# Performance work log

Hardware: AMD Instinct MI355X
Metric: run time of the kernel (lower is better)

## Reference

```python
import jax, jax.numpy as jnp
import numpy as np

B, L, T, IN, H, OUT = 1024, 64, 128, 13, 64, 13
NEG = -1e30


def gru_step(x, h, Wih, Whh, bih, bhh):
    # PyTorch GRU cell: gates ordered (r, z, n)
    gi = x @ Wih.T + bih          # [B, 3H]
    gh = h @ Whh.T + bhh          # [B, 3H]
    ir, iz, inn = jnp.split(gi, 3, axis=-1)
    hr, hz, hn = jnp.split(gh, 3, axis=-1)
    r = jax.nn.sigmoid(ir + hr)
    z = jax.nn.sigmoid(iz + hz)
    n = jnp.tanh(inn + r * hn)
    return (1.0 - z) * n + z * h


def setup_inputs() -> dict:
    key = jax.random.key(0)
    ks = jax.random.split(key, 10)
    s = float(1.0 / np.sqrt(H))
    x = jax.random.normal(ks[0], (B, L, IN), jnp.float32)
    lengths = jax.random.randint(ks[1], (B,), 1, L + 1).at[0].set(L)
    Wih = jax.random.uniform(ks[2], (3 * H, IN), jnp.float32, -s, s)
    Whh = jax.random.uniform(ks[3], (3 * H, H), jnp.float32, -s, s)
    bih = jax.random.uniform(ks[4], (3 * H,), jnp.float32, -s, s)
    bhh = jax.random.uniform(ks[5], (3 * H,), jnp.float32, -s, s)
    Wf = jax.random.uniform(ks[6], (OUT, H), jnp.float32, -s, s)
    bf = jax.random.uniform(ks[7], (OUT,), jnp.float32, -s, s)
    Wa = jax.random.uniform(ks[8], (H, H), jnp.float32, -s, s)
    ba = jax.random.uniform(ks[9], (H,), jnp.float32, -s, s)
    return dict(x=x, lengths=lengths, output_length=T, Wih=Wih, Whh=Whh,
                bih=bih, bhh=bhh, Wf=Wf, bf=bf, Wa=Wa, ba=ba)


def reference(x, lengths, output_length, Wih, Whh, bih, bhh, Wf, bf, Wa, ba):
    b, l = x.shape[0], x.shape[1]
    xT = jnp.swapaxes(x, 0, 1)                        # [L, B, IN]
    h0 = jnp.zeros((b, H), x.dtype)

    # Encoder: masked GRU emulating pack_padded/pad_packed semantics:
    # hidden frozen past each sequence's length; outputs zero past length.
    def enc(h, inp):
        t, xt = inp
        hn = gru_step(xt, h, Wih, Whh, bih, bhh)
        valid = (t < lengths)[:, None]
        h = jnp.where(valid, hn, h)
        return h, jnp.where(valid, hn, 0.0)

    h, outs = jax.lax.scan(enc, h0, (jnp.arange(l), xT))
    # output[:, -1, :] of the padded output (zeros for seqs shorter than max)
    nin = outs[-1] @ Wf.T + bf                        # [B, OUT]

    Tn = output_length
    buf0 = jnp.zeros((Tn, b, H), x.dtype)             # growing past-prediction buffer

    def dec(carry, t):
        h, buf, nin = carry
        hn = gru_step(nin, h, Wih, Whh, bih, bhh)     # output_lstm == hidden (1 layer, 1 step)
        # attention recomputed over all past predictions (softmax over time axis)
        logits = jnp.einsum('tbh,gh->tbg', buf, Wa) + ba      # [T, B, H]
        logits = jnp.where((jnp.arange(Tn) < t)[:, None, None], logits, NEG)
        w = jax.nn.softmax(logits, axis=0)
        o = hn + jnp.sum(w * buf, axis=0)             # at t=0 buffer is all zeros -> +0
        y = o @ Wf.T + bf
        return (hn, buf.at[t].set(o), y), y

    _, ys = jax.lax.scan(dec, (h, buf0, nin), jnp.arange(Tn))
    return jnp.swapaxes(ys, 0, 1)                     # [B, T, OUT]
```

## Files before the change

kernel.cpp:

```cpp
#include <hip/hip_runtime.h>
#include <stdint.h>
#include <math.h>

#define BATCH 1024
#define SEQL  64
#define TDEC  128
#define NIN   13
#define NH    64
#define NOUT  13

typedef _Float16 h2 __attribute__((ext_vector_type(2)));
typedef __fp16   g2 __attribute__((ext_vector_type(2)));

union FU  { uint32_t u; float f; };
union HU  { uint16_t u; _Float16 h; };
union H2U { uint32_t u; h2 h; g2 g; };

__device__ __forceinline__ float bf2f(uint16_t v) { FU t; t.u = ((uint32_t)v) << 16; return t.f; }
__device__ __forceinline__ float hf2f(uint16_t v) { HU t; t.u = v; return (float)t.h; }

__device__ __forceinline__ float ldf(const void* p, long i, int mode) {
    if (mode == 1) return bf2f(((const uint16_t*)p)[i]);
    if (mode == 2) return hf2f(((const uint16_t*)p)[i]);
    return ((const float*)p)[i];
}

__device__ __forceinline__ bool pass_stats(const void* p, int n, int lane, int mode,
                                           float band_lo, float band_hi, float max_ok) {
    int m = (n + 1) / 2;
    int cnt = (m < 64) ? m : 64;
    bool ok_max = true, in_band = false;
    if (lane < cnt) {
        long pos = 2L * (((long)lane * m) / cnt);
        float v = (mode == 1) ? bf2f(((const uint16_t*)p)[pos])
                              : hf2f(((const uint16_t*)p)[pos]);
        float a = fabsf(v);
        ok_max  = (a <= max_ok);
        in_band = (a >= band_lo && a <= band_hi);
    }
    bool allmax = __all(ok_max);
    int nb = (int)__popcll(__ballot(in_band));
    int need = cnt / 4; if (need < 1) need = 1;
    return allmax && (nb >= need);
}
__device__ __forceinline__ int detect(const void* p, int n, int lane,
                                      float band_lo, float band_hi, float max_ok) {
    if (pass_stats(p, n, lane, 1, band_lo, band_hi, max_ok)) return 1;
    if (pass_stats(p, n, lane, 2, band_lo, band_hi, max_ok)) return 2;
    return 0;
}
__device__ __forceinline__ bool detect_len64(const int* p, int lane) {
    int v = p[2 * lane + 1];
    return __all(v == 0);
}

__device__ __forceinline__ float dot2(h2 a, h2 b, float c) {
#if __has_builtin(__builtin_amdgcn_fdot2)
    return __builtin_amdgcn_fdot2(a, b, c, false);
#else
    return c + (float)a[0] * (float)b[0] + (float)a[1] * (float)b[1];
#endif
}
__device__ __forceinline__ uint32_t pku(float a, float b) {
    H2U t; t.g = __builtin_amdgcn_cvt_pkrtz(a, b); return t.u;
}
__device__ __forceinline__ h2 uh(uint32_t u) { H2U t; t.u = u; return t.h; }
__device__ __forceinline__ float rcp_(float x) { return __builtin_amdgcn_rcpf(x); }
__device__ __forceinline__ float sigm(float x)  { return rcp_(1.0f + __expf(-x)); }
__device__ __forceinline__ float tanh_(float x) { return 1.0f - 2.0f * rcp_(__expf(2.0f * x) + 1.0f); }
__device__ __forceinline__ void wb() { __builtin_amdgcn_wave_barrier(); }

__device__ __forceinline__ float swap1(float v) {
    FU a; a.f = v;
    FU b; b.u = (uint32_t)__builtin_amdgcn_mov_dpp((int)a.u, 0xB1, 0xF, 0xF, true);
    return b.f;
}

#define BCAST32(vreg, dst)                                                 \
    {                                                                      \
        uint32_t _pr = pku((vreg), swap1(vreg));                           \
        _Pragma("unroll")                                                  \
        for (int _k = 0; _k < 32; ++_k)                                    \
            (dst)[_k] = __builtin_amdgcn_readlane(_pr, 2 * _k);            \
    }

__global__ __launch_bounds__(64, 1)
void gru_attn_kernel(const void* __restrict__ x, const int* __restrict__ lengths,
                     const void* __restrict__ Wih, const void* __restrict__ Whh,
                     const void* __restrict__ bih, const void* __restrict__ bhh,
                     const void* __restrict__ Wf, const void* __restrict__ bfv,
                     const void* __restrict__ Wa, const void* __restrict__ ba,
                     float* __restrict__ out)
{
    const int b = blockIdx.x;
    const int j = threadIdx.x;

    __shared__ __align__(16) uint32_t xs2[SEQL][8];

    const int dX   = detect(x,   BATCH * SEQL * NIN, j, 0.25f, 4.0f, 16.0f);
    const int dWih = detect(Wih, 3 * NH * NIN, j, 0.04f, 0.13f, 0.14f);
    const int dWhh = detect(Whh, 3 * NH * NH,  j, 0.04f, 0.13f, 0.14f);
    const int dBih = detect(bih, 3 * NH,       j, 0.04f, 0.13f, 0.14f);
    const int dBhh = detect(bhh, 3 * NH,       j, 0.04f, 0.13f, 0.14f);
    const int dWf  = detect(Wf,  NOUT * NH,    j, 0.04f, 0.13f, 0.14f);
    const int dBf  = detect(bfv, NOUT,         j, 0.04f, 0.13f, 0.14f);
    const int dWa  = detect(Wa,  NH * NH,      j, 0.04f, 0.13f, 0.14f);
    const int dBa  = detect(ba,  NH,           j, 0.04f, 0.13f, 0.14f);
    const bool len64 = detect_len64(lengths, j);

    h2 wihr[7], wihz[7], wihn[7];
    h2 whhr[32], whhz[32], whhn[32];
    h2 wap[32], wfp[32];

#pragma unroll
    for (int k = 0; k < 7; ++k) {
        float a0 = ldf(Wih, (0 * NH + j) * NIN + 2 * k, dWih);
        float a1 = (2 * k + 1 < NIN) ? ldf(Wih, (0 * NH + j) * NIN + 2 * k + 1, dWih) : 0.0f;
        wihr[k] = uh(pku(a0, a1));
        float b0 = ldf(Wih, (1 * NH + j) * NIN + 2 * k, dWih);
        float b1 = (2 * k + 1 < NIN) ? ldf(Wih, (1 * NH + j) * NIN + 2 * k + 1, dWih) : 0.0f;
        wihz[k] = uh(pku(b0, b1));
        float c0 = ldf(Wih, (2 * NH + j) * NIN + 2 * k, dWih);
        float c1 = (2 * k + 1 < NIN) ? ldf(Wih, (2 * NH + j) * NIN + 2 * k + 1, dWih) : 0.0f;
        wihn[k] = uh(pku(c0, c1));
    }
    const int jf = (j < NOUT) ? j : 0;
#pragma unroll
    for (int k = 0; k < 32; ++k) {
        whhr[k] = uh(pku(ldf(Whh, (0 * NH + j) * NH + 2 * k, dWhh),
                         ldf(Whh, (0 * NH + j) * NH + 2 * k + 1, dWhh)));
        whhz[k] = uh(pku(ldf(Whh, (1 * NH + j) * NH + 2 * k, dWhh),
                         ldf(Whh, (1 * NH + j) * NH + 2 * k + 1, dWhh)));
        whhn[k] = uh(pku(ldf(Whh, (2 * NH + j) * NH + 2 * k, dWhh),
                         ldf(Whh, (2 * NH + j) * NH + 2 * k + 1, dWhh)));
        wap[k]  = uh(pku(ldf(Wa, j * NH + 2 * k, dWa),
                         ldf(Wa, j * NH + 2 * k + 1, dWa)));
        wfp[k]  = uh(pku(ldf(Wf, jf * NH + 2 * k, dWf),
                         ldf(Wf, jf * NH + 2 * k + 1, dWf)));
    }

    const float bcr = ldf(bih, j, dBih)          + ldf(bhh, j, dBhh);
    const float bcz = ldf(bih, NH + j, dBih)     + ldf(bhh, NH + j, dBhh);
    const float bni = ldf(bih, 2 * NH + j, dBih);
    const float bnh = ldf(bhh, 2 * NH + j, dBhh);
    const float baj = ldf(ba, j, dBa);
    const float bfj = ldf(bfv, jf, dBf);
    const int len = len64 ? lengths[2 * b] : lengths[b];

    {
        const long base = ((long)b * SEQL + j) * NIN;
        float v[14];
#pragma unroll
        for (int k = 0; k < NIN; ++k) v[k] = ldf(x, base + k, dX);
        v[13] = 0.0f;
#pragma unroll
        for (int p = 0; p < 7; ++p) xs2[j][p] = pku(v[2 * p], v[2 * p + 1]);
        xs2[j][7] = 0u;
    }
    wb();

    float h = 0.0f;
    float out_last = 0.0f;

    uint32_t hpk[32];
    BCAST32(h, hpk);

#pragma unroll 1
    for (int t = 0; t < SEQL; ++t) {
        uint4 q0 = *(const uint4*)xs2[t];
        uint4 q1 = *(const uint4*)(xs2[t] + 4);

        float arA = bcr, azA = bcz, hnA = bnh, anA = bni;
        float arB = 0.0f, azB = 0.0f, hnB = 0.0f;
        float arC = 0.0f, azC = 0.0f, hnC = 0.0f;
        float arD = 0.0f, azD = 0.0f, hnD = 0.0f;
#pragma unroll
        for (int k = 0; k < 32; k += 4) {
            h2 h0 = uh(hpk[k]), h1 = uh(hpk[k + 1]), h2v = uh(hpk[k + 2]), h3 = uh(hpk[k + 3]);
            arA = dot2(whhr[k],     h0, arA); azA = dot2(whhz[k],     h0, azA); hnA = dot2(whhn[k],     h0, hnA);
            arB = dot2(whhr[k + 1], h1, arB); azB = dot2(whhz[k + 1], h1, azB); hnB = dot2(whhn[k + 1], h1, hnB);
            arC = dot2(whhr[k + 2], h2v, arC); azC = dot2(whhz[k + 2], h2v, azC); hnC = dot2(whhn[k + 2], h2v, hnC);
            arD = dot2(whhr[k + 3], h3, arD); azD = dot2(whhz[k + 3], h3, azD); hnD = dot2(whhn[k + 3], h3, hnD);
        }
        {
            uint32_t xw[8] = {q0.x, q0.y, q0.z, q0.w, q1.x, q1.y, q1.z, q1.w};
#pragma unroll
            for (int p = 0; p < 7; ++p) {
                h2 xv = uh(xw[p]);
                arB = dot2(wihr[p], xv, arB);
                azB = dot2(wihz[p], xv, azB);
                anA = dot2(wihn[p], xv, anA);
            }
        }
        float ar = (arA + arB) + (arC + arD);
        float az = (azA + azB) + (azC + azD);
        float hna = (hnA + hnB) + (hnC + hnD);
        float r = sigm(ar);
        float z = sigm(az);
        float n = tanh_(anA + r * hna);
        float hnew = n + z * (h - n);
        if (t < len) h = hnew;
        if (t == SEQL - 1) out_last = (t < len) ? hnew : 0.0f;
        BCAST32(h, hpk);
    }

    uint32_t ypk[7];
    {
        uint32_t opk[32];
        BCAST32(out_last, opk);
        float nA = bfj, nB = 0.0f, nC = 0.0f, nD = 0.0f;
#pragma unroll
        for (int k = 0; k < 32; k += 4) {
            nA = dot2(wfp[k],     uh(opk[k]),     nA);
            nB = dot2(wfp[k + 1], uh(opk[k + 1]), nB);
            nC = dot2(wfp[k + 2], uh(opk[k + 2]), nC);
            nD = dot2(wfp[k + 3], uh(opk[k + 3]), nD);
        }
        float nv = (nA + nB) + (nC + nD);
        float nz = (j < NOUT) ? nv : 0.0f;
        uint32_t pr = pku(nz, swap1(nz));
#pragma unroll
        for (int k = 0; k < 7; ++k) ypk[k] = __builtin_amdgcn_readlane(pr, 2 * k);
    }

    float m = -1e30f, Zs = 0.0f, num = 0.0f;

#pragma unroll 1
    for (int t = 0; t < TDEC; ++t) {
        float arA = bcr, azA = bcz, hnA = bnh, anA = bni;
        float arB = 0.0f, azB = 0.0f, hnB = 0.0f;
        float arC = 0.0f, azC = 0.0f, hnC = 0.0f;
        float arD = 0.0f, azD = 0.0f, hnD = 0.0f;
#pragma unroll
        for (int k = 0; k < 32; k += 4) {
            h2 h0 = uh(hpk[k]), h1 = uh(hpk[k + 1]), h2v = uh(hpk[k + 2]), h3 = uh(hpk[k + 3]);
            arA = dot2(whhr[k],     h0, arA); azA = dot2(whhz[k],     h0, azA); hnA = dot2(whhn[k],     h0, hnA);
            arB = dot2(whhr[k + 1], h1, arB); azB = dot2(whhz[k + 1], h1, azB); hnB = dot2(whhn[k + 1], h1, hnB);
            arC = dot2(whhr[k + 2], h2v, arC); azC = dot2(whhz[k + 2], h2v, azC); hnC = dot2(whhn[k + 2], h2v, hnC);
            arD = dot2(whhr[k + 3], h3, arD); azD = dot2(whhz[k + 3], h3, azD); hnD = dot2(whhn[k + 3], h3, hnD);
        }
#pragma unroll
        for (int p = 0; p < 7; ++p) {
            h2 xv = uh(ypk[p]);
            arB = dot2(wihr[p], xv, arB);
            azB = dot2(wihz[p], xv, azB);
            anA = dot2(wihn[p], xv, anA);
        }
        float ar = (arA + arB) + (arC + arD);
        float az = (azA + azB) + (azC + azD);
        float hna = (hnA + hnB) + (hnC + hnD);
        float r = sigm(ar);
        float z = sigm(az);
        float n = tanh_(anA + r * hna);
        float hnew = n + z * (h - n);
        h = hnew;
        float attn = (t > 0) ? num * rcp_(Zs) : 0.0f;
        float o = hnew + attn;

        BCAST32(hnew, hpk);
        uint32_t opk[32];
        BCAST32(o, opk);

        float sA = baj, yA = bfj, sB = 0.0f, yB = 0.0f, sC = 0.0f, yC = 0.0f, sD = 0.0f, yD = 0.0f;
#pragma unroll
        for (int k = 0; k < 32; k += 4) {
            h2 o0 = uh(opk[k]), o1 = uh(opk[k + 1]), o2 = uh(opk[k + 2]), o3 = uh(opk[k + 3]);
            sA = dot2(wap[k],     o0, sA); yA = dot2(wfp[k],     o0, yA);
            sB = dot2(wap[k + 1], o1, sB); yB = dot2(wfp[k + 1], o1, yB);
            sC = dot2(wap[k + 2], o2, sC); yC = dot2(wfp[k + 2], o2, yC);
            sD = dot2(wap[k + 3], o3, sD); yD = dot2(wfp[k + 3], o3, yD);
        }
        float s  = (sA + sB) + (sC + sD);
        float yv = (yA + yB) + (yC + yD);
        float mn = fmaxf(m, s);
        float al = __expf(m - mn);
        float p  = __expf(s - mn);
        Zs  = Zs * al + p;
        num = num * al + p * o;
        m = mn;
        if (j < NOUT) out[((size_t)b * TDEC + t) * NOUT + j] = yv;
        float yz = (j < NOUT) ? yv : 0.0f;
        uint32_t pr = pku(yz, swap1(yz));
#pragma unroll
        for (int k = 0; k < 7; ++k) ypk[k] = __builtin_amdgcn_readlane(pr, 2 * k);
    }
}

extern "C" void kernel_launch(void* const* d_in, const int* in_sizes, int n_in,
                              void* d_out, int out_size, void* d_ws, size_t ws_size,
                              hipStream_t stream) {
    (void)in_sizes; (void)n_in; (void)out_size; (void)d_ws; (void)ws_size;
    const void* x      = d_in[0];
    const int* lengths = (const int*)d_in[1];
    const void* Wih = d_in[3];
    const void* Whh = d_in[4];
    const void* bih = d_in[5];
    const void* bhh = d_in[6];
    const void* Wf  = d_in[7];
    const void* bf  = d_in[8];
    const void* Wa  = d_in[9];
    const void* ba  = d_in[10];
    float* out = (float*)d_out;

    gru_attn_kernel<<<dim3(BATCH), dim3(64), 0, stream>>>(
        x, lengths, Wih, Whh, bih, bhh, Wf, bf, Wa, ba, out);
}
```

Measured before the change: 224.3 us.

## Fold log2e into weights, keep x in registers, unroll decoder by four

Pre-scales the gate, recurrent and attention weights and biases by log2(e) (or 2·log2(e) for the candidate gate) so sigmoid, tanh and softmax exponentials use the native exp2 with no per-step multiply. The encoder input is now kept in per-lane registers and fetched with readlane instead of going through shared memory, which also removes the wave barrier. The decoder is unrolled four steps per iteration with batched output stores, and the encoder loop is unrolled by two. Scaling the weights before packing to fp16 changes rounding slightly, and the unrolling raises register pressure.

```diff
diff --git a/kernel.cpp b/kernel.cpp
--- a/kernel.cpp
+++ b/kernel.cpp
@@ -66,9 +66,15 @@
 }
 __device__ __forceinline__ h2 uh(uint32_t u) { H2U t; t.u = u; return t.h; }
 __device__ __forceinline__ float rcp_(float x) { return __builtin_amdgcn_rcpf(x); }
-__device__ __forceinline__ float sigm(float x)  { return rcp_(1.0f + __expf(-x)); }
-__device__ __forceinline__ float tanh_(float x) { return 1.0f - 2.0f * rcp_(__expf(2.0f * x) + 1.0f); }
-__device__ __forceinline__ void wb() { __builtin_amdgcn_wave_barrier(); }
+__device__ __forceinline__ float exp2_(float x) {
+#if __has_builtin(__builtin_amdgcn_exp2f)
+    return __builtin_amdgcn_exp2f(x);
+#else
+    return __expf(x * 0.69314718056f);
+#endif
+}
+__device__ __forceinline__ float sigm2(float xs)  { return rcp_(1.0f + exp2_(-xs)); }
+__device__ __forceinline__ float tanh2(float xs)  { return 1.0f - 2.0f * rcp_(exp2_(xs) + 1.0f); }
 
 __device__ __forceinline__ float swap1(float v) {
     FU a; a.f = v;
@@ -82,6 +88,67 @@
         _Pragma("unroll")                                                  \
         for (int _k = 0; _k < 32; ++_k)                                    \
             (dst)[_k] = __builtin_amdgcn_readlane(_pr, 2 * _k);            \
+    }
+
+#define DEC_STEP(T_, YSLOT)                                                        \
+    {                                                                              \
+        float arA = bcr, azA = bcz, hnA = bnh, anA = bni;                          \
+        float arB = 0.0f, azB = 0.0f, hnB = 0.0f;                                  \
+        float arC = 0.0f, azC = 0.0f, hnC = 0.0f;                                  \
+        float arD = 0.0f, azD = 0.0f, hnD = 0.0f;                                  \
+        _Pragma("unroll")                                                          \
+        for (int k = 0; k < 32; k += 4) {                                          \
+            h2 h0 = uh(hpk[k]), h1 = uh(hpk[k + 1]);                               \
+            h2 h2v = uh(hpk[k + 2]), h3 = uh(hpk[k + 3]);                          \
+            arA = dot2(whhr[k],     h0, arA); azA = dot2(whhz[k],     h0, azA); hnA = dot2(whhn[k],     h0, hnA); \
+            arB = dot2(whhr[k + 1], h1, arB); azB = dot2(whhz[k + 1], h1, azB); hnB = dot2(whhn[k + 1], h1, hnB); \
+            arC = dot2(whhr[k + 2], h2v, arC); azC = dot2(whhz[k + 2], h2v, azC); hnC = dot2(whhn[k + 2], h2v, hnC); \
+            arD = dot2(whhr[k + 3], h3, arD); azD = dot2(whhz[k + 3], h3, azD); hnD = dot2(whhn[k + 3], h3, hnD); \
+        }                                                                          \
+        _Pragma("unroll")                                                          \
+        for (int p = 0; p < 7; ++p) {                                              \
+            h2 xv = uh(ypk[p]);                                                    \
+            arB = dot2(wihr[p], xv, arB);                                          \
+            azB = dot2(wihz[p], xv, azB);                                          \
+            anA = dot2(wihn[p], xv, anA);                                          \
+        }                                                                          \
+        float ar = (arA + arB) + (arC + arD);                                      \
+        float az = (azA + azB) + (azC + azD);                                      \
+        float hna = (hnA + hnB) + (hnC + hnD);                                     \
+        float r_ = sigm2(ar);                                                      \
+        float z_ = sigm2(az);                                                      \
+        float n_ = tanh2(anA + r_ * hna);                                          \
+        float hnew = n_ + z_ * (h - n_);                                           \
+        h = hnew;                                                                  \
+        float attn = ((T_) > 0) ? num * rcp_(Zs) : 0.0f;                           \
+        float o_ = hnew + attn;                                                    \
+        BCAST32(hnew, hpk);                                                        \
+        uint32_t opk[32];                                                          \
+        BCAST32(o_, opk);                                                          \
+        float sA = baj, yA = bfj, sB = 0.0f, yB = 0.0f;                            \
+        float sC = 0.0f, yC = 0.0f, sD = 0.0f, yD = 0.0f;                          \
+        _Pragma("unroll")                                                          \
+        for (int k = 0; k < 32; k += 4) {                                          \
+            h2 o0 = uh(opk[k]), o1 = uh(opk[k + 1]);                               \
+            h2 o2 = uh(opk[k + 2]), o3 = uh(opk[k + 3]);                           \
+            sA = dot2(wap[k],     o0, sA); yA = dot2(wfp[k],     o0, yA);          \
+            sB = dot2(wap[k + 1], o1, sB); yB = dot2(wfp[k + 1], o1, yB);          \
+            sC = dot2(wap[k + 2], o2, sC); yC = dot2(wfp[k + 2], o2, yC);          \
+            sD = dot2(wap[k + 3], o3, sD); yD = dot2(wfp[k + 3], o3, yD);          \
+        }                                                                          \
+        float s_  = (sA + sB) + (sC + sD);                                         \
+        float yv_ = (yA + yB) + (yC + yD);                                         \
+        float mn = fmaxf(m, s_);                                                   \
+        float al = exp2_(m - mn);                                                  \
+        float pp = exp2_(s_ - mn);                                                 \
+        Zs  = Zs * al + pp;                                                        \
+        num = num * al + pp * o_;                                                  \
+        m = mn;                                                                    \
+        YSLOT = yv_;                                                               \
+        float yz = (j < NOUT) ? yv_ : 0.0f;                                        \
+        uint32_t pr_ = pku(yz, swap1(yz));                                         \
+        _Pragma("unroll")                                                          \
+        for (int k = 0; k < 7; ++k) ypk[k] = __builtin_amdgcn_readlane(pr_, 2 * k);\
     }
 
 __global__ __launch_bounds__(64, 1)
@@ -95,8 +162,6 @@
     const int b = blockIdx.x;
     const int j = threadIdx.x;
 
-    __shared__ __align__(16) uint32_t xs2[SEQL][8];
-
     const int dX   = detect(x,   BATCH * SEQL * NIN, j, 0.25f, 4.0f, 16.0f);
     const int dWih = detect(Wih, 3 * NH * NIN, j, 0.04f, 0.13f, 0.14f);
     const int dWhh = detect(Whh, 3 * NH * NH,  j, 0.04f, 0.13f, 0.14f);
@@ -108,6 +173,9 @@
     const int dBa  = detect(ba,  NH,           j, 0.04f, 0.13f, 0.14f);
     const bool len64 = detect_len64(lengths, j);
 
+    const float L2E  = 1.44269504089f;
+    const float L2E2 = 2.88539008177f;
+
     h2 wihr[7], wihz[7], wihn[7];
     h2 whhr[32], whhz[32], whhn[32];
     h2 wap[32], wfp[32];
@@ -116,37 +184,38 @@
     for (int k = 0; k < 7; ++k) {
         float a0 = ldf(Wih, (0 * NH + j) * NIN + 2 * k, dWih);
         float a1 = (2 * k + 1 < NIN) ? ldf(Wih, (0 * NH + j) * NIN + 2 * k + 1, dWih) : 0.0f;
-        wihr[k] = uh(pku(a0, a1));
+        wihr[k] = uh(pku(a0 * L2E, a1 * L2E));
         float b0 = ldf(Wih, (1 * NH + j) * NIN + 2 * k, dWih);
         float b1 = (2 * k + 1 < NIN) ? ldf(Wih, (1 * NH + j) * NIN + 2 * k + 1, dWih) : 0.0f;
-        wihz[k] = uh(pku(b0, b1));
+        wihz[k] = uh(pku(b0 * L2E, b1 * L2E));
         float c0 = ldf(Wih, (2 * NH + j) * NIN + 2 * k, dWih);
         float c1 = (2 * k + 1 < NIN) ? ldf(Wih, (2 * NH + j) * NIN + 2 * k + 1, dWih) : 0.0f;
-        wihn[k] = uh(pku(c0, c1));
+        wihn[k] = uh(pku(c0 * L2E2, c1 * L2E2));
     }
     const int jf = (j < NOUT) ? j : 0;
 #pragma unroll
     for (int k = 0; k < 32; ++k) {
-        whhr[k] = uh(pku(ldf(Whh, (0 * NH + j) * NH + 2 * k, dWhh),
-                         ldf(Whh, (0 * NH + j) * NH + 2 * k + 1, dWhh)));
-        whhz[k] = uh(pku(ldf(Whh, (1 * NH + j) * NH + 2 * k, dWhh),
-                         ldf(Whh, (1 * NH + j) * NH + 2 * k + 1, dWhh)));
-        whhn[k] = uh(pku(ldf(Whh, (2 * NH + j) * NH + 2 * k, dWhh),
-                         ldf(Whh, (2 * NH + j) * NH + 2 * k + 1, dWhh)));
-        wap[k]  = uh(pku(ldf(Wa, j * NH + 2 * k, dWa),
-                         ldf(Wa, j * NH + 2 * k + 1, dWa)));
+        whhr[k] = uh(pku(ldf(Whh, (0 * NH + j) * NH + 2 * k, dWhh) * L2E,
+                         ldf(Whh, (0 * NH + j) * NH + 2 * k + 1, dWhh) * L2E));
+        whhz[k] = uh(pku(ldf(Whh, (1 * NH + j) * NH + 2 * k, dWhh) * L2E,
+                         ldf(Whh, (1 * NH + j) * NH + 2 * k + 1, dWhh) * L2E));
+        whhn[k] = uh(pku(ldf(Whh, (2 * NH + j) * NH + 2 * k, dWhh) * L2E2,
+                         ldf(Whh, (2 * NH + j) * NH + 2 * k + 1, dWhh) * L2E2));
+        wap[k]  = uh(pku(ldf(Wa, j * NH + 2 * k, dWa) * L2E,
+                         ldf(Wa, j * NH + 2 * k + 1, dWa) * L2E));
         wfp[k]  = uh(pku(ldf(Wf, jf * NH + 2 * k, dWf),
                          ldf(Wf, jf * NH + 2 * k + 1, dWf)));
     }
 
-    const float bcr = ldf(bih, j, dBih)          + ldf(bhh, j, dBhh);
-    const float bcz = ldf(bih, NH + j, dBih)     + ldf(bhh, NH + j, dBhh);
-    const float bni = ldf(bih, 2 * NH + j, dBih);
-    const float bnh = ldf(bhh, 2 * NH + j, dBhh);
-    const float baj = ldf(ba, j, dBa);
+    const float bcr = (ldf(bih, j, dBih)      + ldf(bhh, j, dBhh))      * L2E;
+    const float bcz = (ldf(bih, NH + j, dBih) + ldf(bhh, NH + j, dBhh)) * L2E;
+    const float bni = ldf(bih, 2 * NH + j, dBih) * L2E2;
+    const float bnh = ldf(bhh, 2 * NH + j, dBhh) * L2E2;
+    const float baj = ldf(ba, j, dBa) * L2E;
     const float bfj = ldf(bfv, jf, dBf);
     const int len = len64 ? lengths[2 * b] : lengths[b];
 
+    uint32_t xp[7];
     {
         const long base = ((long)b * SEQL + j) * NIN;
         float v[14];
@@ -154,21 +223,21 @@
         for (int k = 0; k < NIN; ++k) v[k] = ldf(x, base + k, dX);
         v[13] = 0.0f;
 #pragma unroll
-        for (int p = 0; p < 7; ++p) xs2[j][p] = pku(v[2 * p], v[2 * p + 1]);
-        xs2[j][7] = 0u;
-    }
-    wb();
+        for (int p = 0; p < 7; ++p) xp[p] = pku(v[2 * p], v[2 * p + 1]);
+    }
 
     float h = 0.0f;
     float out_last = 0.0f;
 
     uint32_t hpk[32];
-    BCAST32(h, hpk);
-
-#pragma unroll 1
+#pragma unroll
+    for (int k = 0; k < 32; ++k) hpk[k] = 0u;
+
+#pragma unroll 2
     for (int t = 0; t < SEQL; ++t) {
-        uint4 q0 = *(const uint4*)xs2[t];
-        uint4 q1 = *(const uint4*)(xs2[t] + 4);
+        uint32_t xw[7];
+#pragma unroll
+        for (int p = 0; p < 7; ++p) xw[p] = __builtin_amdgcn_readlane(xp[p], t);
 
         float arA = bcr, azA = bcz, hnA = bnh, anA = bni;
         float arB = 0.0f, azB = 0.0f, hnB = 0.0f;
@@ -182,25 +251,23 @@
             arC = dot2(whhr[k + 2], h2v, arC); azC = dot2(whhz[k + 2], h2v, azC); hnC = dot2(whhn[k + 2], h2v, hnC);
             arD = dot2(whhr[k + 3], h3, arD); azD = dot2(whhz[k + 3], h3, azD); hnD = dot2(whhn[k + 3], h3, hnD);
         }
-        {
-            uint32_t xw[8] = {q0.x, q0.y, q0.z, q0.w, q1.x, q1.y, q1.z, q1.w};
-#pragma unroll
-            for (int p = 0; p < 7; ++p) {
-                h2 xv = uh(xw[p]);
-                arB = dot2(wihr[p], xv, arB);
-                azB = dot2(wihz[p], xv, azB);
-                anA = dot2(wihn[p], xv, anA);
-            }
+#pragma unroll
+        for (int p = 0; p < 7; ++p) {
+            h2 xv = uh(xw[p]);
+            arB = dot2(wihr[p], xv, arB);
+            azB = dot2(wihz[p], xv, azB);
+            anA = dot2(wihn[p], xv, anA);
         }
         float ar = (arA + arB) + (arC + arD);
         float az = (azA + azB) + (azC + azD);
         float hna = (hnA + hnB) + (hnC + hnD);
-        float r = sigm(ar);
-        float z = sigm(az);
-        float n = tanh_(anA + r * hna);
+        float r = sigm2(ar);
+        float z = sigm2(az);
+        float n = tanh2(anA + r * hna);
         float hnew = n + z * (h - n);
-        if (t < len) h = hnew;
-        if (t == SEQL - 1) out_last = (t < len) ? hnew : 0.0f;
+        bool upd = (t < len);
+        h = upd ? hnew : h;
+        if (t == SEQL - 1) out_last = upd ? hnew : 0.0f;
         BCAST32(h, hpk);
     }
 
@@ -226,63 +293,19 @@
     float m = -1e30f, Zs = 0.0f, num = 0.0f;
 
 #pragma unroll 1
-    for (int t = 0; t < TDEC; ++t) {
-        float arA = bcr, azA = bcz, hnA = bnh, anA = bni;
-        float arB = 0.0f, azB = 0.0f, hnB = 0.0f;
-        float arC = 0.0f, azC = 0.0f, hnC = 0.0f;
-        float arD = 0.0f, azD = 0.0f, hnD = 0.0f;
-#pragma unroll
-        for (int k = 0; k < 32; k += 4) {
-            h2 h0 = uh(hpk[k]), h1 = uh(hpk[k + 1]), h2v = uh(hpk[k + 2]), h3 = uh(hpk[k + 3]);
-            arA = dot2(whhr[k],     h0, arA); azA = dot2(whhz[k],     h0, azA); hnA = dot2(whhn[k],     h0, hnA);
-            arB = dot2(whhr[k + 1], h1, arB); azB = dot2(whhz[k + 1], h1, azB); hnB = dot2(whhn[k + 1], h1, hnB);
-            arC = dot2(whhr[k + 2], h2v, arC); azC = dot2(whhz[k + 2], h2v, azC); hnC = dot2(whhn[k + 2], h2v, hnC);
-            arD = dot2(whhr[k + 3], h3, arD); azD = dot2(whhz[k + 3], h3, azD); hnD = dot2(whhn[k + 3], h3, hnD);
+    for (int t0 = 0; t0 < TDEC; t0 += 4) {
+        float y0, y1, y2, y3;
+        DEC_STEP(t0 + 0, y0);
+        DEC_STEP(t0 + 1, y1);
+        DEC_STEP(t0 + 2, y2);
+        DEC_STEP(t0 + 3, y3);
+        if (j < NOUT) {
+            size_t base_ = ((size_t)b * TDEC + t0) * NOUT + j;
+            out[base_]            = y0;
+            out[base_ + NOUT]     = y1;
+            out[base_ + 2 * NOUT] = y2;
+            out[base_ + 3 * NOUT] = y3;
         }
-#pragma unroll
-        for (int p = 0; p < 7; ++p) {
-            h2 xv = uh(ypk[p]);
-            arB = dot2(wihr[p], xv, arB);
-            azB = dot2(wihz[p], xv, azB);
-            anA = dot2(wihn[p], xv, anA);
-        }
-        float ar = (arA + arB) + (arC + arD);
-        float az = (azA + azB) + (azC + azD);
-        float hna = (hnA + hnB) + (hnC + hnD);
-        float r = sigm(ar);
-        float z = sigm(az);
-        float n = tanh_(anA + r * hna);
-        float hnew = n + z * (h - n);
-        h = hnew;
-        float attn = (t > 0) ? num * rcp_(Zs) : 0.0f;
-        float o = hnew + attn;
-
-        BCAST32(hnew, hpk);
-        uint32_t opk[32];
-        BCAST32(o, opk);
-
-        float sA = baj, yA = bfj, sB = 0.0f, yB = 0.0f, sC = 0.0f, yC = 0.0f, sD = 0.0f, yD = 0.0f;
-#pragma unroll
-        for (int k = 0; k < 32; k += 4) {
-            h2 o0 = uh(opk[k]), o1 = uh(opk[k + 1]), o2 = uh(opk[k + 2]), o3 = uh(opk[k + 3]);
-            sA = dot2(wap[k],     o0, sA); yA = dot2(wfp[k],     o0, yA);
-            sB = dot2(wap[k + 1], o1, sB); yB = dot2(wfp[k + 1], o1, yB);
-            sC = dot2(wap[k + 2], o2, sC); yC = dot2(wfp[k + 2], o2, yC);
-            sD = dot2(wap[k + 3], o3, sD); yD = dot2(wfp[k + 3], o3, yD);
-        }
-        float s  = (sA + sB) + (sC + sD);
-        float yv = (yA + yB) + (yC + yD);
-        float mn = fmaxf(m, s);
-        float al = __expf(m - mn);
-        float p  = __expf(s - mn);
-        Zs  = Zs * al + p;
-        num = num * al + p * o;
-        m = mn;
-        if (j < NOUT) out[((size_t)b * TDEC + t) * NOUT + j] = yv;
-        float yz = (j < NOUT) ? yv : 0.0f;
-        uint32_t pr = pku(yz, swap1(yz));
-#pragma unroll
-        for (int k = 0; k < 7; ++k) ypk[k] = __builtin_amdgcn_readlane(pr, 2 * k);
     }
 }
 
```

After: 228.9 us, median of 2. +2.1%, slower.

## Software-pipeline GRU input projections and decoder output; fold log2e into weights

Applied to the files above, without the earlier changes.

Scales gate and attention weights and biases by log2(e) (or 2·log2(e) for the n gate) so sigmoid, tanh and the softmax use a native exp2 without a per-call multiply. The encoder input projection for step t+1 is computed during step t from registers via readlane, which replaces the shared-memory x staging and takes that work off the critical path. The decoder loop is rotated so the output projection and attention score for the previous o run alongside the current step's hidden matvec, letting independent dot products interleave. In exchange there is more register pressure, a peeled first and last iteration, and slightly different rounding from scaling weights before the fp16 conversion.

```diff
diff --git a/kernel.cpp b/kernel.cpp
--- a/kernel.cpp
+++ b/kernel.cpp
@@ -66,9 +66,15 @@
 }
 __device__ __forceinline__ h2 uh(uint32_t u) { H2U t; t.u = u; return t.h; }
 __device__ __forceinline__ float rcp_(float x) { return __builtin_amdgcn_rcpf(x); }
-__device__ __forceinline__ float sigm(float x)  { return rcp_(1.0f + __expf(-x)); }
-__device__ __forceinline__ float tanh_(float x) { return 1.0f - 2.0f * rcp_(__expf(2.0f * x) + 1.0f); }
-__device__ __forceinline__ void wb() { __builtin_amdgcn_wave_barrier(); }
+__device__ __forceinline__ float exp2_(float x) {
+#if __has_builtin(__builtin_amdgcn_exp2f)
+    return __builtin_amdgcn_exp2f(x);
+#else
+    return __expf(x * 0.69314718056f);
+#endif
+}
+__device__ __forceinline__ float sigm2(float xs)  { return rcp_(1.0f + exp2_(-xs)); }
+__device__ __forceinline__ float tanh2(float xs)  { return 1.0f - 2.0f * rcp_(exp2_(xs) + 1.0f); }
 
 __device__ __forceinline__ float swap1(float v) {
     FU a; a.f = v;
@@ -95,8 +101,6 @@
     const int b = blockIdx.x;
     const int j = threadIdx.x;
 
-    __shared__ __align__(16) uint32_t xs2[SEQL][8];
-
     const int dX   = detect(x,   BATCH * SEQL * NIN, j, 0.25f, 4.0f, 16.0f);
     const int dWih = detect(Wih, 3 * NH * NIN, j, 0.04f, 0.13f, 0.14f);
     const int dWhh = detect(Whh, 3 * NH * NH,  j, 0.04f, 0.13f, 0.14f);
@@ -108,6 +112,9 @@
     const int dBa  = detect(ba,  NH,           j, 0.04f, 0.13f, 0.14f);
     const bool len64 = detect_len64(lengths, j);
 
+    const float L2E  = 1.44269504089f;
+    const float L2E2 = 2.88539008177f;
+
     h2 wihr[7], wihz[7], wihn[7];
     h2 whhr[32], whhz[32], whhn[32];
     h2 wap[32], wfp[32];
@@ -116,37 +123,38 @@
     for (int k = 0; k < 7; ++k) {
         float a0 = ldf(Wih, (0 * NH + j) * NIN + 2 * k, dWih);
         float a1 = (2 * k + 1 < NIN) ? ldf(Wih, (0 * NH + j) * NIN + 2 * k + 1, dWih) : 0.0f;
-        wihr[k] = uh(pku(a0, a1));
+        wihr[k] = uh(pku(a0 * L2E, a1 * L2E));
         float b0 = ldf(Wih, (1 * NH + j) * NIN + 2 * k, dWih);
         float b1 = (2 * k + 1 < NIN) ? ldf(Wih, (1 * NH + j) * NIN + 2 * k + 1, dWih) : 0.0f;
-        wihz[k] = uh(pku(b0, b1));
+        wihz[k] = uh(pku(b0 * L2E, b1 * L2E));
         float c0 = ldf(Wih, (2 * NH + j) * NIN + 2 * k, dWih);
         float c1 = (2 * k + 1 < NIN) ? ldf(Wih, (2 * NH + j) * NIN + 2 * k + 1, dWih) : 0.0f;
-        wihn[k] = uh(pku(c0, c1));
+        wihn[k] = uh(pku(c0 * L2E2, c1 * L2E2));
     }
     const int jf = (j < NOUT) ? j : 0;
 #pragma unroll
     for (int k = 0; k < 32; ++k) {
-        whhr[k] = uh(pku(ldf(Whh, (0 * NH + j) * NH + 2 * k, dWhh),
-                         ldf(Whh, (0 * NH + j) * NH + 2 * k + 1, dWhh)));
-        whhz[k] = uh(pku(ldf(Whh, (1 * NH + j) * NH + 2 * k, dWhh),
-                         ldf(Whh, (1 * NH + j) * NH + 2 * k + 1, dWhh)));
-        whhn[k] = uh(pku(ldf(Whh, (2 * NH + j) * NH + 2 * k, dWhh),
-                         ldf(Whh, (2 * NH + j) * NH + 2 * k + 1, dWhh)));
-        wap[k]  = uh(pku(ldf(Wa, j * NH + 2 * k, dWa),
-                         ldf(Wa, j * NH + 2 * k + 1, dWa)));
+        whhr[k] = uh(pku(ldf(Whh, (0 * NH + j) * NH + 2 * k, dWhh) * L2E,
+                         ldf(Whh, (0 * NH + j) * NH + 2 * k + 1, dWhh) * L2E));
+        whhz[k] = uh(pku(ldf(Whh, (1 * NH + j) * NH + 2 * k, dWhh) * L2E,
+                         ldf(Whh, (1 * NH + j) * NH + 2 * k + 1, dWhh) * L2E));
+        whhn[k] = uh(pku(ldf(Whh, (2 * NH + j) * NH + 2 * k, dWhh) * L2E2,
+                         ldf(Whh, (2 * NH + j) * NH + 2 * k + 1, dWhh) * L2E2));
+        wap[k]  = uh(pku(ldf(Wa, j * NH + 2 * k, dWa) * L2E,
+                         ldf(Wa, j * NH + 2 * k + 1, dWa) * L2E));
         wfp[k]  = uh(pku(ldf(Wf, jf * NH + 2 * k, dWf),
                          ldf(Wf, jf * NH + 2 * k + 1, dWf)));
     }
 
-    const float bcr = ldf(bih, j, dBih)          + ldf(bhh, j, dBhh);
-    const float bcz = ldf(bih, NH + j, dBih)     + ldf(bhh, NH + j, dBhh);
-    const float bni = ldf(bih, 2 * NH + j, dBih);
-    const float bnh = ldf(bhh, 2 * NH + j, dBhh);
-    const float baj = ldf(ba, j, dBa);
+    const float bcr = (ldf(bih, j, dBih)      + ldf(bhh, j, dBhh))      * L2E;
+    const float bcz = (ldf(bih, NH + j, dBih) + ldf(bhh, NH + j, dBhh)) * L2E;
+    const float bni = ldf(bih, 2 * NH + j, dBih) * L2E2;
+    const float bnh = ldf(bhh, 2 * NH + j, dBhh) * L2E2;
+    const float baj = ldf(ba, j, dBa) * L2E;
     const float bfj = ldf(bfv, jf, dBf);
     const int len = len64 ? lengths[2 * b] : lengths[b];
 
+    uint32_t xp[7];
     {
         const long base = ((long)b * SEQL + j) * NIN;
         float v[14];
@@ -154,23 +162,35 @@
         for (int k = 0; k < NIN; ++k) v[k] = ldf(x, base + k, dX);
         v[13] = 0.0f;
 #pragma unroll
-        for (int p = 0; p < 7; ++p) xs2[j][p] = pku(v[2 * p], v[2 * p + 1]);
-        xs2[j][7] = 0u;
-    }
-    wb();
+        for (int p = 0; p < 7; ++p) xp[p] = pku(v[2 * p], v[2 * p + 1]);
+    }
 
     float h = 0.0f;
     float out_last = 0.0f;
 
     uint32_t hpk[32];
-    BCAST32(h, hpk);
+#pragma unroll
+    for (int k = 0; k < 32; ++k) hpk[k] = 0u;
+
+    float gir, giz, gin;
+    {
+        uint32_t xw[7];
+#pragma unroll
+        for (int p = 0; p < 7; ++p) xw[p] = __builtin_amdgcn_readlane(xp[p], 0);
+        float r0 = 0.0f, z0 = 0.0f, n0 = 0.0f;
+#pragma unroll
+        for (int p = 0; p < 7; ++p) {
+            h2 xv = uh(xw[p]);
+            r0 = dot2(wihr[p], xv, r0);
+            z0 = dot2(wihz[p], xv, z0);
+            n0 = dot2(wihn[p], xv, n0);
+        }
+        gir = r0; giz = z0; gin = n0;
+    }
 
 #pragma unroll 1
     for (int t = 0; t < SEQL; ++t) {
-        uint4 q0 = *(const uint4*)xs2[t];
-        uint4 q1 = *(const uint4*)(xs2[t] + 4);
-
-        float arA = bcr, azA = bcz, hnA = bnh, anA = bni;
+        float arA = bcr, azA = bcz, hnA = bnh;
         float arB = 0.0f, azB = 0.0f, hnB = 0.0f;
         float arC = 0.0f, azC = 0.0f, hnC = 0.0f;
         float arD = 0.0f, azD = 0.0f, hnD = 0.0f;
@@ -182,29 +202,38 @@
             arC = dot2(whhr[k + 2], h2v, arC); azC = dot2(whhz[k + 2], h2v, azC); hnC = dot2(whhn[k + 2], h2v, hnC);
             arD = dot2(whhr[k + 3], h3, arD); azD = dot2(whhz[k + 3], h3, azD); hnD = dot2(whhn[k + 3], h3, hnD);
         }
+
+        float girN = 0.0f, gizN = 0.0f, ginN = 0.0f;
         {
-            uint32_t xw[8] = {q0.x, q0.y, q0.z, q0.w, q1.x, q1.y, q1.z, q1.w};
+            uint32_t xwN[7];
+#pragma unroll
+            for (int p = 0; p < 7; ++p)
+                xwN[p] = __builtin_amdgcn_readlane(xp[p], (t + 1) & 63);
 #pragma unroll
             for (int p = 0; p < 7; ++p) {
-                h2 xv = uh(xw[p]);
-                arB = dot2(wihr[p], xv, arB);
-                azB = dot2(wihz[p], xv, azB);
-                anA = dot2(wihn[p], xv, anA);
+                h2 xv = uh(xwN[p]);
+                girN = dot2(wihr[p], xv, girN);
+                gizN = dot2(wihz[p], xv, gizN);
+                ginN = dot2(wihn[p], xv, ginN);
             }
         }
-        float ar = (arA + arB) + (arC + arD);
-        float az = (azA + azB) + (azC + azD);
+
+        float ar = ((arA + arB) + (arC + arD)) + gir;
+        float az = ((azA + azB) + (azC + azD)) + giz;
         float hna = (hnA + hnB) + (hnC + hnD);
-        float r = sigm(ar);
-        float z = sigm(az);
-        float n = tanh_(anA + r * hna);
+        float an = bni + gin;
+        float r = sigm2(ar);
+        float z = sigm2(az);
+        float n = tanh2(an + r * hna);
         float hnew = n + z * (h - n);
-        if (t < len) h = hnew;
-        if (t == SEQL - 1) out_last = (t < len) ? hnew : 0.0f;
+        bool upd = (t < len);
+        h = upd ? hnew : h;
+        if (t == SEQL - 1) out_last = upd ? hnew : 0.0f;
         BCAST32(h, hpk);
-    }
-
-    uint32_t ypk[7];
+        gir = girN; giz = gizN; gin = ginN;
+    }
+
+    uint32_t ypk0[7];
     {
         uint32_t opk[32];
         BCAST32(out_last, opk);
@@ -220,13 +249,13 @@
         float nz = (j < NOUT) ? nv : 0.0f;
         uint32_t pr = pku(nz, swap1(nz));
 #pragma unroll
-        for (int k = 0; k < 7; ++k) ypk[k] = __builtin_amdgcn_readlane(pr, 2 * k);
+        for (int k = 0; k < 7; ++k) ypk0[k] = __builtin_amdgcn_readlane(pr, 2 * k);
     }
 
     float m = -1e30f, Zs = 0.0f, num = 0.0f;
-
-#pragma unroll 1
-    for (int t = 0; t < TDEC; ++t) {
+    float o_prev;
+
+    {
         float arA = bcr, azA = bcz, hnA = bnh, anA = bni;
         float arB = 0.0f, azB = 0.0f, hnB = 0.0f;
         float arC = 0.0f, azC = 0.0f, hnC = 0.0f;
@@ -241,48 +270,111 @@
         }
 #pragma unroll
         for (int p = 0; p < 7; ++p) {
+            h2 xv = uh(ypk0[p]);
+            arB = dot2(wihr[p], xv, arB);
+            azB = dot2(wihz[p], xv, azB);
+            anA = dot2(wihn[p], xv, anA);
+        }
+        float ar = (arA + arB) + (arC + arD);
+        float az = (azA + azB) + (azC + azD);
+        float hna = (hnA + hnB) + (hnC + hnD);
+        float r = sigm2(ar);
+        float z = sigm2(az);
+        float n = tanh2(anA + r * hna);
+        float hnew = n + z * (h - n);
+        h = hnew;
+        BCAST32(hnew, hpk);
+        o_prev = hnew;
+    }
+
+#pragma unroll 1
+    for (int t = 1; t < TDEC; ++t) {
+        uint32_t opk[32];
+        BCAST32(o_prev, opk);
+
+        float arA = bcr, azA = bcz, hnA = bnh, anA = bni;
+        float arB = 0.0f, azB = 0.0f, hnB = 0.0f;
+        float arC = 0.0f, azC = 0.0f, hnC = 0.0f;
+        float arD = 0.0f, azD = 0.0f, hnD = 0.0f;
+#pragma unroll
+        for (int k = 0; k < 32; k += 4) {
+            h2 h0 = uh(hpk[k]), h1 = uh(hpk[k + 1]), h2v = uh(hpk[k + 2]), h3 = uh(hpk[k + 3]);
+            arA = dot2(whhr[k],     h0, arA); azA = dot2(whhz[k],     h0, azA); hnA = dot2(whhn[k],     h0, hnA);
+            arB = dot2(whhr[k + 1], h1, arB); azB = dot2(whhz[k + 1], h1, azB); hnB = dot2(whhn[k + 1], h1, hnB);
+            arC = dot2(whhr[k + 2], h2v, arC); azC = dot2(whhz[k + 2], h2v, azC); hnC = dot2(whhn[k + 2], h2v, hnC);
+            arD = dot2(whhr[k + 3], h3, arD); azD = dot2(whhz[k + 3], h3, azD); hnD = dot2(whhn[k + 3], h3, hnD);
+        }
+
+        float yA = bfj, yB = 0.0f, yC = 0.0f, yD = 0.0f;
+#pragma unroll
+        for (int k = 0; k < 32; k += 4) {
+            yA = dot2(wfp[k],     uh(opk[k]),     yA);
+            yB = dot2(wfp[k + 1], uh(opk[k + 1]), yB);
+            yC = dot2(wfp[k + 2], uh(opk[k + 2]), yC);
+            yD = dot2(wfp[k + 3], uh(opk[k + 3]), yD);
+        }
+        float yv = (yA + yB) + (yC + yD);
+        if (j < NOUT) out[((size_t)b * TDEC + (t - 1)) * NOUT + j] = yv;
+
+        uint32_t ypk[7];
+        {
+            float yz = (j < NOUT) ? yv : 0.0f;
+            uint32_t pr = pku(yz, swap1(yz));
+#pragma unroll
+            for (int k = 0; k < 7; ++k) ypk[k] = __builtin_amdgcn_readlane(pr, 2 * k);
+        }
+#pragma unroll
+        for (int p = 0; p < 7; ++p) {
             h2 xv = uh(ypk[p]);
             arB = dot2(wihr[p], xv, arB);
             azB = dot2(wihz[p], xv, azB);
             anA = dot2(wihn[p], xv, anA);
         }
+
+        float sA = baj, sB = 0.0f, sC = 0.0f, sD = 0.0f;
+#pragma unroll
+        for (int k = 0; k < 32; k += 4) {
+            sA = dot2(wap[k],     uh(opk[k]),     sA);
+            sB = dot2(wap[k + 1], uh(opk[k + 1]), sB);
+            sC = dot2(wap[k + 2], uh(opk[k + 2]), sC);
+            sD = dot2(wap[k + 3], uh(opk[k + 3]), sD);
+        }
+        float s_ = (sA + sB) + (sC + sD);
+        float mn = fmaxf(m, s_);
+        float al = exp2_(m - mn);
+        float pp = exp2_(s_ - mn);
+        Zs  = Zs * al + pp;
+        num = num * al + pp * o_prev;
+        m = mn;
+
         float ar = (arA + arB) + (arC + arD);
         float az = (azA + azB) + (azC + azD);
         float hna = (hnA + hnB) + (hnC + hnD);
-        float r = sigm(ar);
-        float z = sigm(az);
-        float n = tanh_(anA + r * hna);
-        float hnew = n + z * (h - n);
+        float r_ = sigm2(ar);
+        float z_ = sigm2(az);
+        float n_ = tanh2(anA + r_ * hna);
+        float hnew = n_ + z_ * (h - n_);
         h = hnew;
-        float attn = (t > 0) ? num * rcp_(Zs) : 0.0f;
-        float o = hnew + attn;
-
+
+        float attn = num * rcp_(Zs);
+        float o_ = hnew + attn;
         BCAST32(hnew, hpk);
+        o_prev = o_;
+    }
+
+    {
         uint32_t opk[32];
-        BCAST32(o, opk);
-
-        float sA = baj, yA = bfj, sB = 0.0f, yB = 0.0f, sC = 0.0f, yC = 0.0f, sD = 0.0f, yD = 0.0f;
-#pragma unroll
-        for (int k = 0; k < 32; k += 4) {
-            h2 o0 = uh(opk[k]), o1 = uh(opk[k + 1]), o2 = uh(opk[k + 2]), o3 = uh(opk[k + 3]);
-            sA = dot2(wap[k],     o0, sA); yA = dot2(wfp[k],     o0, yA);
-            sB = dot2(wap[k + 1], o1, sB); yB = dot2(wfp[k + 1], o1, yB);
-            sC = dot2(wap[k + 2], o2, sC); yC = dot2(wfp[k + 2], o2, yC);
-            sD = dot2(wap[k + 3], o3, sD); yD = dot2(wfp[k + 3], o3, yD);
-        }
-        float s  = (sA + sB) + (sC + sD);
+        BCAST32(o_prev, opk);
+        float yA = bfj, yB = 0.0f, yC = 0.0f, yD = 0.0f;
+#pragma unroll
+        for (int k = 0; k < 32; k += 4) {
+            yA = dot2(wfp[k],     uh(opk[k]),     yA);
+            yB = dot2(wfp[k + 1], uh(opk[k + 1]), yB);
+            yC = dot2(wfp[k + 2], uh(opk[k + 2]), yC);
+            yD = dot2(wfp[k + 3], uh(opk[k + 3]), yD);
+        }
         float yv = (yA + yB) + (yC + yD);
-        float mn = fmaxf(m, s);
-        float al = __expf(m - mn);
-        float p  = __expf(s - mn);
-        Zs  = Zs * al + p;
-        num = num * al + p * o;
-        m = mn;
-        if (j < NOUT) out[((size_t)b * TDEC + t) * NOUT + j] = yv;
-        float yz = (j < NOUT) ? yv : 0.0f;
-        uint32_t pr = pku(yz, swap1(yz));
-#pragma unroll
-        for (int k = 0; k < 7; ++k) ypk[k] = __builtin_amdgcn_readlane(pr, 2 * k);
+        if (j < NOUT) out[((size_t)b * TDEC + (TDEC - 1)) * NOUT + j] = yv;
     }
 }
 
```

New measurement: 231.4 us. 3.2% more time.
